# Kernel optimization log

Measured on AMD Instinct MI355X. Metric: run time of the kernel, lower is better.

## Reference

```python
import jax, jax.numpy as jnp
import numpy as np

D_IN = 1024
D_OUT = 1024
NUM_HEADS = 16
HEAD_DIM = D_OUT // NUM_HEADS


def setup_inputs() -> dict:
    key = jax.random.key(0)
    ks = jax.random.split(key, 6)
    scale = 0.02
    x = jax.random.normal(ks[0], (8, 1024, D_IN), dtype=jnp.float32)
    # weights stored as [in, out] (transposed vs torch Linear.weight)
    W_query = jax.random.normal(ks[1], (D_IN, D_OUT), dtype=jnp.float32) * scale
    W_key = jax.random.normal(ks[2], (D_IN, HEAD_DIM), dtype=jnp.float32) * scale
    W_value = jax.random.normal(ks[3], (D_IN, HEAD_DIM), dtype=jnp.float32) * scale
    W_out = jax.random.normal(ks[4], (D_OUT, D_OUT), dtype=jnp.float32) * scale
    b_out = jax.random.normal(ks[5], (D_OUT,), dtype=jnp.float32) * scale
    return {"x": x, "W_query": W_query, "W_key": W_key, "W_value": W_value,
            "W_out": W_out, "b_out": b_out}


def reference(x, W_query, W_key, W_value, W_out, b_out):
    B, S, _ = x.shape
    H, Dh = NUM_HEADS, HEAD_DIM
    q = (x @ W_query).reshape(B, S, H, Dh).transpose(0, 2, 1, 3)  # [B,H,S,Dh]
    k = x @ W_key      # [B,S,Dh] single shared head
    v = x @ W_value    # [B,S,Dh]
    # scores: broadcast shared K across all query heads (no explicit repeat)
    scores = jnp.einsum("bhqd,bkd->bhqk", q, k)  # [B,H,S,S]
    causal = jnp.triu(jnp.ones((S, S), dtype=bool), k=1)
    scores = jnp.where(causal[None, None], -jnp.inf, scores)
    attn = jax.nn.softmax(scores / np.sqrt(Dh).astype(np.float32), axis=-1)
    # dropout p=0.0 -> identity
    ctx = jnp.einsum("bhqk,bkd->bhqd", attn, v)  # [B,H,S,Dh]
    ctx = ctx.transpose(0, 2, 1, 3).reshape(B, S, H * Dh)
    return ctx @ W_out + b_out
```

## Files before the change

### kernel.cpp

```cpp
#include <hip/hip_runtime.h>

typedef unsigned short u16;
typedef __attribute__((ext_vector_type(8))) short short8;
typedef __attribute__((ext_vector_type(4))) float f32x4;
typedef __attribute__((ext_vector_type(16))) float f32x16;
typedef __attribute__((ext_vector_type(4))) unsigned short u16x4;
typedef __attribute__((ext_vector_type(4))) int i32x4;

__device__ __forceinline__ u16 f2b(float f) {
  unsigned u = __float_as_uint(f);
  unsigned r = (u + 0x7fffu + ((u >> 16) & 1u)) >> 16;
  return (u16)r;
}

__device__ __forceinline__ void gload16(const u16* g, u16* l) {
  __builtin_amdgcn_global_load_lds((const __attribute__((address_space(1))) void*)g,
                                   (__attribute__((address_space(3))) void*)l, 16, 0, 0);
}

__global__ void prep(const float* __restrict__ x, const float* __restrict__ Wq,
                     const float* __restrict__ Wk, const float* __restrict__ Wv,
                     const float* __restrict__ Wo, u16* __restrict__ xb,
                     u16* __restrict__ wqT, u16* __restrict__ wkT,
                     u16* __restrict__ wvT, u16* __restrict__ woT) {
  __shared__ float t[32][33];
  int bid = blockIdx.x;
  if (bid < 8192) {
    const int i = (bid * 256 + threadIdx.x) * 4;
    f32x4 v = *(const f32x4*)(x + i);
    u16x4 o;
    o[0] = f2b(v[0]); o[1] = f2b(v[1]); o[2] = f2b(v[2]); o[3] = f2b(v[3]);
    *(u16x4*)(xb + i) = o;
    return;
  }
  bid -= 8192;
  const float* in; u16* out; int C, bx, by;
  if (bid < 1024)      { in = Wq; out = wqT; C = 1024; bx = bid & 31; by = bid >> 5; }
  else if (bid < 1088) { in = Wk; out = wkT; C = 64;   bid -= 1024; bx = bid & 1; by = bid >> 1; }
  else if (bid < 1152) { in = Wv; out = wvT; C = 64;   bid -= 1088; bx = bid & 1; by = bid >> 1; }
  else                 { in = Wo; out = woT; C = 1024; bid -= 1152; bx = bid & 31; by = bid >> 5; }
  const int R = 1024;
  const int c0 = bx * 32, r0 = by * 32;
  const int tx = threadIdx.x & 31, ty = threadIdx.x >> 5;
#pragma unroll
  for (int i = 0; i < 32; i += 8)
    t[ty + i][tx] = in[(size_t)(r0 + ty + i) * C + c0 + tx];
  __syncthreads();
#pragma unroll
  for (int i = 0; i < 32; i += 8)
    out[(size_t)(c0 + ty + i) * R + r0 + tx] = f2b(t[tx][ty + i]);
}

#define GEMM_CORE(A_PTR, B_PTR)                                                        \
  __shared__ u16 As[4096];                                                \
  __shared__ u16 Bs[8192];                                               \
  const int tid = threadIdx.x;                                                         \
  const int lane = tid & 63, wid = tid >> 6;                              \
  const int lg = lane >> 4, li = lane & 15;                                            \
  const int wr = wid >> 1, wc = wid & 1;                                               \
  f32x4 acc[2][4] = {};                                                                \
  const int lrow = lane >> 3, lslot = lane & 7;                                        \
  const int scol = 8 * (lslot ^ lrow);                    \
  const u16* Ab = (A_PTR) + (size_t)(m0 + wid * 16 + lrow) * 1024 + scol;              \
  const u16* Bb = (B_PTR) + (size_t)(wid * 32 + lrow) * 1024 + scol;                   \
  u16* const dA = As + wid * 1024;                                                     \
  u16* const dB = Bs + wid * 2048;                                                     \
  for (int t = 0; t < 16; ++t) {                                                       \
    const int k0 = t * 64;                                                             \
    __syncthreads();                                                                   \
    gload16(Ab + k0,        dA);                                                       \
    gload16(Ab + k0 + 8192, dA + 512);                                                 \
    _Pragma("unroll")                                                                  \
    for (int c_ = 0; c_ < 4; ++c_) gload16(Bb + k0 + c_ * 8192, dB + c_ * 512);        \
    __syncthreads();                                                                   \
    _Pragma("unroll")                                                                  \
    for (int kki = 0; kki < 2; ++kki) {                                                \
      short8 af[2], bfr[4];                                                            \
      _Pragma("unroll")                                                                \
      for (int mi = 0; mi < 2; ++mi) {                                                 \
        const int r = wr * 32 + mi * 16 + li;                                          \
        af[mi] = *(const short8*)&As[r * 64 + 8 * ((4 * kki + lg) ^ (r & 7))];         \
      }                                                                                \
      _Pragma("unroll")                                                                \
      for (int ni = 0; ni < 4; ++ni) {                                                 \
        const int r = wc * 64 + ni * 16 + li;                                          \
        bfr[ni] = *(const short8*)&Bs[r * 64 + 8 * ((4 * kki + lg) ^ (r & 7))];        \
      }                                                                                \
      _Pragma("unroll")                                                                \
      for (int mi = 0; mi < 2; ++mi)                                                   \
        _Pragma("unroll")                                                              \
        for (int ni = 0; ni < 4; ++ni)                                                 \
          acc[mi][ni] =                                                                \
              __builtin_amdgcn_mfma_f32_16x16x32_bf16(af[mi], bfr[ni], acc[mi][ni],    \
                                                      0, 0, 0);                        \
    }                                                                                  \
  }

__global__ __launch_bounds__(256) void gemm_proj(
    const u16* __restrict__ A, const u16* __restrict__ BtQ, const u16* __restrict__ BtKV,
    u16* __restrict__ Qp, u16* __restrict__ K3, u16* __restrict__ Vt3, float scaleQ) {
  const int m0 = blockIdx.x * 64;
  const int by = blockIdx.y;
  const bool isQ = (by < 8);
  const int n0 = isQ ? by * 128 : 0;
  GEMM_CORE(A, (isQ ? BtQ + (size_t)n0 * 1024 : BtKV))

#pragma unroll
  for (int mi = 0; mi < 2; ++mi) {
#pragma unroll
    for (int ni = 0; ni < 4; ++ni) {
      const int n = n0 + wc * 64 + ni * 16 + li;
#pragma unroll
      for (int i = 0; i < 4; ++i) {
        const int m = m0 + wr * 32 + mi * 16 + lg * 4 + i;
        const float v = acc[mi][ni][i];
        const int bb = m >> 10, ss = m & 1023;
        const int qt = ss >> 5, sl = ss & 31;
        if (isQ) {
          const int h = n >> 6, dd = n & 63;
          const int t = dd >> 4, h2 = (dd >> 3) & 1, j = dd & 7;
          Qp[(((((size_t)bb * 16 + h) * 32 + qt) * 4 + t) * 2 + h2) * 256 + sl * 8 + j] =
              f2b(v * scaleQ);
        } else if (n < 64) {
          const int t = n >> 4, h2 = (n >> 3) & 1, j = n & 7;
          K3[(((((size_t)bb * 32 + qt) * 4 + t) * 2 + h2) * 32 + sl) * 8 + j] = f2b(v);
        } else {
          const int d = n - 64;
          const int ks = sl >> 4, rem = sl & 15;
          const int h2 = (rem >> 2) & 1, j = (rem & 3) | ((rem >> 3) << 2);
          Vt3[(((((size_t)bb * 32 + qt) * 2 + ks) * 2 + h2) * 64 + d) * 8 + j] = f2b(v);
        }
      }
    }
  }
}

__global__ __launch_bounds__(256) void gemm_out(
    const u16* __restrict__ A, const u16* __restrict__ Bt,
    float* __restrict__ Cf, const float* __restrict__ bias) {
  const int m0 = blockIdx.x * 64;
  const int n0 = blockIdx.y * 128;
  GEMM_CORE(A, Bt + (size_t)n0 * 1024)

#pragma unroll
  for (int mi = 0; mi < 2; ++mi)
#pragma unroll
    for (int ni = 0; ni < 4; ++ni) {
      const int n = n0 + wc * 64 + ni * 16 + li;
#pragma unroll
      for (int i = 0; i < 4; ++i) {
        const int m = m0 + wr * 32 + mi * 16 + lg * 4 + i;
        Cf[(size_t)m * 1024 + n] = acc[mi][ni][i] + bias[n];
      }
    }
}

__global__ __launch_bounds__(256, 4) void attn_mqa8(
    const u16* __restrict__ qp, const u16* __restrict__ k3,
    const u16* __restrict__ vt3, u16* __restrict__ ctxb) {
  __shared__ __align__(16) u16 smem[16384];
  const int lane = threadIdx.x & 63, wid = threadIdx.x >> 6;
  const int bx = blockIdx.x;
  const int qt = 31 - (bx >> 6);
  const int r6 = bx & 63;
  const int b  = r6 >> 3;
  const int hp = r6 & 7;
  const int hh = wid & 1;
  const int s  = wid >> 1;
  const int h  = hp * 2 + hh;
  const int l31 = lane & 31, hi = lane >> 5;
  const int n0t = (qt + 2) >> 1;
  const int cs  = s ? (qt + 1 - n0t) : n0t;
  const int base = s ? n0t : 0;
  const int task = (b * 16 + h) * 32 + qt;

  const u16* k3b = k3 + (size_t)b * 65536;
  const u16* v3b = vt3 + (size_t)b * 65536;
  const int sreg = s * 4096;
  const int doff = hh * 1024;
  const int loff = lane * 8;

  const u16* qbase = qp + (size_t)task * 2048 + hi * 256 + l31 * 8;
  short8 qa[4];
#pragma unroll
  for (int t = 0; t < 4; ++t) qa[t] = *(const short8*)(qbase + t * 512);

  f32x16 acc0 = {}, acc1 = {};
  float lsum = 0.f;

  if (cs > 0) {
    const size_t o = (size_t)base * 2048 + doff + loff;
    gload16(k3b + o,       &smem[sreg + doff]);
    gload16(k3b + o + 512, &smem[sreg + doff + 512]);
    gload16(v3b + o,       &smem[8192 + sreg + doff]);
    gload16(v3b + o + 512, &smem[8192 + sreg + doff + 512]);
  }
  __syncthreads();

  int par = 0;
  for (int i = 0; i < n0t; ++i, par ^= 1) {
    if (i + 1 < cs) {
      const size_t o = (size_t)(base + i + 1) * 2048 + doff + loff;
      const int dst = sreg + (par ^ 1) * 2048 + doff;
      gload16(k3b + o,       &smem[dst]);
      gload16(k3b + o + 512, &smem[dst + 512]);
      gload16(v3b + o,       &smem[8192 + dst]);
      gload16(v3b + o + 512, &smem[8192 + dst + 512]);
    }
    if (i < cs) {
      const int kvt = base + i;
      const u16* lkb = &smem[sreg + par * 2048];
      const u16* lvb = &smem[8192 + sreg + par * 2048];
      short8 kc[4];
#pragma unroll
      for (int t = 0; t < 4; ++t)
        kc[t] = *(const short8*)&lkb[l31 * 8 + (t * 2 + hi) * 256];
      const u16* vtt = &lvb[hi * 512 + l31 * 8];
      const short8 vf0 = *(const short8*)(vtt);
      const short8 vf1 = *(const short8*)(vtt + 1024);
      const short8 vf2 = *(const short8*)(vtt + 256);
      const short8 vf3 = *(const short8*)(vtt + 1280);

      f32x16 st = {};
#pragma unroll
      for (int t = 0; t < 4; ++t)
        st = __builtin_amdgcn_mfma_f32_32x32x16_bf16(kc[t], qa[t], st, 0, 0, 0);

      if (kvt == qt) {
#pragma unroll
        for (int r = 0; r < 16; ++r) {
          const int crow = (r & 3) + 8 * (r >> 2) + 4 * hi;
          if (crow > l31) st[r] = -1e38f;
        }
      }
      float e[16];
#pragma unroll
      for (int r = 0; r < 16; ++r)
        asm("v_exp_f32 %0, %1" : "=v"(e[r]) : "v"(st[r]));
      lsum += ((e[0] + e[1]) + (e[2] + e[3])) + ((e[4] + e[5]) + (e[6] + e[7])) +
              (((e[8] + e[9]) + (e[10] + e[11])) + ((e[12] + e[13]) + (e[14] + e[15])));

      unsigned pw0, pw1, pw2, pw3, pw4, pw5, pw6, pw7;
      asm("v_cvt_pk_bf16_f32 %0, %1, %2" : "=v"(pw0) : "v"(e[0]),  "v"(e[1]));
      asm("v_cvt_pk_bf16_f32 %0, %1, %2" : "=v"(pw1) : "v"(e[2]),  "v"(e[3]));
      asm("v_cvt_pk_bf16_f32 %0, %1, %2" : "=v"(pw2) : "v"(e[4]),  "v"(e[5]));
      asm("v_cvt_pk_bf16_f32 %0, %1, %2" : "=v"(pw3) : "v"(e[6]),  "v"(e[7]));
      asm("v_cvt_pk_bf16_f32 %0, %1, %2" : "=v"(pw4) : "v"(e[8]),  "v"(e[9]));
      asm("v_cvt_pk_bf16_f32 %0, %1, %2" : "=v"(pw5) : "v"(e[10]), "v"(e[11]));
      asm("v_cvt_pk_bf16_f32 %0, %1, %2" : "=v"(pw6) : "v"(e[12]), "v"(e[13]));
      asm("v_cvt_pk_bf16_f32 %0, %1, %2" : "=v"(pw7) : "v"(e[14]), "v"(e[15]));
      i32x4 w0 = {(int)pw0, (int)pw1, (int)pw2, (int)pw3};
      i32x4 w1 = {(int)pw4, (int)pw5, (int)pw6, (int)pw7};
      const short8 pa0 = *(const short8*)&w0;
      const short8 pa1 = *(const short8*)&w1;

      acc0 = __builtin_amdgcn_mfma_f32_32x32x16_bf16(pa0, vf0, acc0, 0, 0, 0);
      acc0 = __builtin_amdgcn_mfma_f32_32x32x16_bf16(pa1, vf1, acc0, 0, 0, 0);
      acc1 = __builtin_amdgcn_mfma_f32_32x32x16_bf16(pa0, vf2, acc1, 0, 0, 0);
      acc1 = __builtin_amdgcn_mfma_f32_32x32x16_bf16(pa1, vf3, acc1, 0, 0, 0);
    }
    __syncthreads();
  }

  const float lfull = lsum + __shfl_xor(lsum, 32, 64);
  float* exf = (float*)smem;
  if (s == 1) {
    float* ab = exf + hh * 2048 + lane * 32;
#pragma unroll
    for (int r = 0; r < 16; ++r) {
      ab[(2 * r) ^ (lane & 31)] = acc0[r];
      ab[(2 * r + 1) ^ (lane & 31)] = acc1[r];
    }
    exf[4096 + hh * 64 + lane] = lfull;
  }
  __syncthreads();
  if (s == 0) {
    const float lfp = exf[4096 + hh * 64 + lane];
    const float linv = 1.0f / (lfull + lfp);
    const float* ab = exf + hh * 2048 + lane * 32;
#pragma unroll
    for (int r = 0; r < 16; ++r) {
      const int crow = (r & 3) + 8 * (r >> 2) + 4 * hi;
      const float lr = __shfl(linv, crow, 64);
      const float o0 = acc0[r] + ab[(2 * r) ^ (lane & 31)];
      const float o1 = acc1[r] + ab[(2 * r + 1) ^ (lane & 31)];
      const size_t mrow = (size_t)(b * 1024 + qt * 32 + crow) * 1024 + h * 64;
      ctxb[mrow + l31] = f2b(o0 * lr);
      ctxb[mrow + 32 + l31] = f2b(o1 * lr);
    }
  }
}

extern "C" void kernel_launch(void* const* d_in, const int* in_sizes, int n_in,
                              void* d_out, int out_size, void* d_ws, size_t ws_size,
                              hipStream_t stream) {
  const float* x  = (const float*)d_in[0];
  const float* Wq = (const float*)d_in[1];
  const float* Wk = (const float*)d_in[2];
  const float* Wv = (const float*)d_in[3];
  const float* Wo = (const float*)d_in[4];
  const float* bo = (const float*)d_in[5];
  float* out = (float*)d_out;

  u16* ws16 = (u16*)d_ws;
  const size_t M1 = 1u << 20;
  u16* woT  = ws16;
  u16* qp   = ws16 + 1 * M1;
  u16* k3   = ws16 + 9 * M1;
  u16* vt3  = ws16 + 9 * M1 + (M1 >> 1);
  u16* xb   = ws16 + 10 * M1;
  u16* ctx  = ws16 + 10 * M1;
  u16* wqT  = ws16 + 18 * M1;
  u16* wkT  = ws16 + 19 * M1;
  u16* wvT  = wkT + 65536;

  prep<<<10368, 256, 0, stream>>>(x, Wq, Wk, Wv, Wo, xb, wqT, wkT, wvT, woT);

  const float SCL = 0.125f * 1.44269504088896340736f;
  gemm_proj<<<dim3(128, 9), 256, 0, stream>>>(xb, wqT, wkT, qp, k3, vt3, SCL);

  attn_mqa8<<<2048, 256, 0, stream>>>(qp, k3, vt3, ctx);

  gemm_out<<<dim3(128, 8), 256, 0, stream>>>(ctx, woT, out, bo);
}
```

Measured before the change: 100.6 us.

## Share each K/V tile across four heads per block and swizzle GEMM block order

The attention kernel now runs 512-thread blocks covering four query heads instead of two, so each shared K/V tile loaded into LDS serves twice as many heads. Each wave issues half as many global-to-LDS loads and the grid shrinks to 1024 blocks. Both GEMM kernels also remap block IDs so consecutive blocks stride across the N dimension, which is meant to improve L2 reuse of the A and B tiles. The larger blocks use more LDS and registers per block, which may reduce occupancy or scheduling flexibility.

Result: slower. 102.8 us (+2.2%).

```diff
diff --git a/kernel.cpp b/kernel.cpp
--- a/kernel.cpp
+++ b/kernel.cpp
@@ -99,10 +99,12 @@
 __global__ __launch_bounds__(256) void gemm_proj(
     const u16* __restrict__ A, const u16* __restrict__ BtQ, const u16* __restrict__ BtKV,
     u16* __restrict__ Qp, u16* __restrict__ K3, u16* __restrict__ Vt3, float scaleQ) {
-  const int m0 = blockIdx.x * 64;
-  const int by = blockIdx.y;
-  const bool isQ = (by < 8);
-  const int n0 = isQ ? by * 128 : 0;
+  const int bid = blockIdx.y * 128 + blockIdx.x;
+  const int nb = (bid & 7) * 144 + (bid >> 3);
+  const int m0 = (nb & 127) * 64;
+  const int sby = nb >> 7;
+  const bool isQ = (sby < 8);
+  const int n0 = isQ ? sby * 128 : 0;
   GEMM_CORE(A, (isQ ? BtQ + (size_t)n0 * 1024 : BtKV))
 
 #pragma unroll
@@ -138,8 +140,10 @@
 __global__ __launch_bounds__(256) void gemm_out(
     const u16* __restrict__ A, const u16* __restrict__ Bt,
     float* __restrict__ Cf, const float* __restrict__ bias) {
-  const int m0 = blockIdx.x * 64;
-  const int n0 = blockIdx.y * 128;
+  const int bid = blockIdx.y * 128 + blockIdx.x;
+  const int nb = (bid & 7) * 128 + (bid >> 3);
+  const int m0 = (nb & 127) * 64;
+  const int n0 = (nb >> 7) * 128;
   GEMM_CORE(A, Bt + (size_t)n0 * 1024)
 
 #pragma unroll
@@ -155,19 +159,19 @@
     }
 }
 
-__global__ __launch_bounds__(256, 4) void attn_mqa8(
+__global__ __launch_bounds__(512) void attn_mqa9(
     const u16* __restrict__ qp, const u16* __restrict__ k3,
     const u16* __restrict__ vt3, u16* __restrict__ ctxb) {
-  __shared__ __align__(16) u16 smem[16384];
+  __shared__ __align__(16) u16 smem[16896];
   const int lane = threadIdx.x & 63, wid = threadIdx.x >> 6;
   const int bx = blockIdx.x;
-  const int qt = 31 - (bx >> 6);
-  const int r6 = bx & 63;
-  const int b  = r6 >> 3;
-  const int hp = r6 & 7;
-  const int hh = wid & 1;
-  const int s  = wid >> 1;
-  const int h  = hp * 2 + hh;
+  const int qt = 31 - (bx >> 5);
+  const int r5 = bx & 31;
+  const int b  = r5 >> 2;
+  const int hq = r5 & 3;
+  const int hh = wid & 3;
+  const int s  = wid >> 2;
+  const int h  = hq * 4 + hh;
   const int l31 = lane & 31, hi = lane >> 5;
   const int n0t = (qt + 2) >> 1;
   const int cs  = s ? (qt + 1 - n0t) : n0t;
@@ -177,7 +181,7 @@
   const u16* k3b = k3 + (size_t)b * 65536;
   const u16* v3b = vt3 + (size_t)b * 65536;
   const int sreg = s * 4096;
-  const int doff = hh * 1024;
+  const int doff = hh * 512;
   const int loff = lane * 8;
 
   const u16* qbase = qp + (size_t)task * 2048 + hi * 256 + l31 * 8;
@@ -190,10 +194,8 @@
 
   if (cs > 0) {
     const size_t o = (size_t)base * 2048 + doff + loff;
-    gload16(k3b + o,       &smem[sreg + doff]);
-    gload16(k3b + o + 512, &smem[sreg + doff + 512]);
-    gload16(v3b + o,       &smem[8192 + sreg + doff]);
-    gload16(v3b + o + 512, &smem[8192 + sreg + doff + 512]);
+    gload16(k3b + o, &smem[sreg + doff]);
+    gload16(v3b + o, &smem[8192 + sreg + doff]);
   }
   __syncthreads();
 
@@ -202,10 +204,8 @@
     if (i + 1 < cs) {
       const size_t o = (size_t)(base + i + 1) * 2048 + doff + loff;
       const int dst = sreg + (par ^ 1) * 2048 + doff;
-      gload16(k3b + o,       &smem[dst]);
-      gload16(k3b + o + 512, &smem[dst + 512]);
-      gload16(v3b + o,       &smem[8192 + dst]);
-      gload16(v3b + o + 512, &smem[8192 + dst + 512]);
+      gload16(k3b + o, &smem[dst]);
+      gload16(v3b + o, &smem[8192 + dst]);
     }
     if (i < cs) {
       const int kvt = base + i;
@@ -271,11 +271,11 @@
       ab[(2 * r) ^ (lane & 31)] = acc0[r];
       ab[(2 * r + 1) ^ (lane & 31)] = acc1[r];
     }
-    exf[4096 + hh * 64 + lane] = lfull;
+    exf[8192 + hh * 64 + lane] = lfull;
   }
   __syncthreads();
   if (s == 0) {
-    const float lfp = exf[4096 + hh * 64 + lane];
+    const float lfp = exf[8192 + hh * 64 + lane];
     const float linv = 1.0f / (lfull + lfp);
     const float* ab = exf + hh * 2048 + lane * 32;
 #pragma unroll
@@ -319,7 +319,7 @@
   const float SCL = 0.125f * 1.44269504088896340736f;
   gemm_proj<<<dim3(128, 9), 256, 0, stream>>>(xb, wqT, wkT, qp, k3, vt3, SCL);
 
-  attn_mqa8<<<2048, 256, 0, stream>>>(qp, k3, vt3, ctx);
+  attn_mqa9<<<1024, 512, 0, stream>>>(qp, k3, vt3, ctx);
 
   gemm_out<<<dim3(128, 8), 256, 0, stream>>>(ctx, woT, out, bo);
 }
```
